# Performance work log

Hardware: AMD Instinct MI355X
Metric: run time of the kernel (lower is better)

## Reference

```python
import jax, jax.numpy as jnp
import numpy as np

IN_CAP_N = 1152   # 128*3*3
IN_CAP_SZ = 5
OUT_CAP_N = 55
OUT_CAP_SZ = 1
BATCH = 8192
ROUTING_ITERS = 2


def setup_inputs() -> dict:
    key = jax.random.key(0)
    k_u, k_w = jax.random.split(key)
    u = jax.random.normal(k_u, (BATCH, IN_CAP_SZ, 128, 3, 3), dtype=jnp.float32)
    W = jax.random.normal(k_w, (1, IN_CAP_N, OUT_CAP_SZ), dtype=jnp.float32)
    b = jnp.zeros((OUT_CAP_N, OUT_CAP_SZ), dtype=jnp.float32)
    return {"u": u, "W": W, "b": b}


def _squash(s):
    # s: (B, 55, 1)
    norm_sq = jnp.sum(s * s, axis=2, keepdims=True)
    norm = jnp.sqrt(norm_sq)
    return norm / (1.0 + norm_sq) * s


def reference(u, W, b):
    B = u.shape[0]
    u_ = u.reshape(B, IN_CAP_SZ, IN_CAP_N)              # (B, 5, 1152)
    u_hat = jnp.matmul(u_, jnp.broadcast_to(W, (B, IN_CAP_N, OUT_CAP_SZ)))  # (B, 5, 1)
    # routing logits, expanded from (55,1) param to (B, 55, 5)
    b_ij = jnp.broadcast_to(b, (B, OUT_CAP_N, IN_CAP_SZ))
    v = None
    for _ in range(ROUTING_ITERS):
        c = jax.nn.softmax(b_ij, axis=1)                 # softmax over out-capsules
        s = jnp.matmul(c, u_hat)                         # (B, 55, 5)@(B, 5, 1) -> (B, 55, 1)
        v = _squash(s)
        b_ij = b_ij + jnp.matmul(v, jnp.swapaxes(u_hat, 1, 2))  # (B, 55, 5)
    return v
```

## Files before the change

kernel.cpp:

```cpp
#include <hip/hip_runtime.h>
#include <math.h>

#define IN_CAP_N   1152
#define IN_CAP_SZ  5
#define OUT_CAP_N  55
#define NBATCH     8192

__global__ __launch_bounds__(320) void digitcaps_kernel(
    const float* __restrict__ u,
    const float* __restrict__ W,
    const float* __restrict__ bparam,
    float* __restrict__ out)
{
    __shared__ float sW[IN_CAP_N];
    __shared__ float s_uhat[IN_CAP_SZ];

    const int tid  = threadIdx.x;
    const int wave = tid >> 6;
    const int lane = tid & 63;
    const int b    = blockIdx.x;

    if (tid < IN_CAP_N / 4) {
        ((float4*)sW)[tid] = ((const float4*)W)[tid];
    }
    __syncthreads();

    const float* urow = u + ((size_t)b * IN_CAP_SZ + wave) * IN_CAP_N;
    float acc = 0.f;
    #pragma unroll
    for (int p = 0; p < 4; ++p) {
        int f = p * 64 + lane;
        float4 uv = ((const float4*)urow)[f];
        float4 wv = ((const float4*)sW)[f];
        acc += uv.x * wv.x + uv.y * wv.y + uv.z * wv.z + uv.w * wv.w;
    }
    if (lane < 32) {
        int f = 256 + lane;
        float4 uv = ((const float4*)urow)[f];
        float4 wv = ((const float4*)sW)[f];
        acc += uv.x * wv.x + uv.y * wv.y + uv.z * wv.z + uv.w * wv.w;
    }
    #pragma unroll
    for (int off = 32; off > 0; off >>= 1)
        acc += __shfl_down(acc, off, 64);
    if (lane == 0) s_uhat[wave] = acc;
    __syncthreads();

    if (wave == 0) {
        float h[IN_CAP_SZ];
        #pragma unroll
        for (int i = 0; i < IN_CAP_SZ; ++i) h[i] = s_uhat[i];

        const bool active = (lane < OUT_CAP_N);
        float binit = active ? bparam[lane] : 0.f;
        float bij[IN_CAP_SZ];
        #pragma unroll
        for (int i = 0; i < IN_CAP_SZ; ++i) bij[i] = binit;

        float v = 0.f;
        #pragma unroll
        for (int it = 0; it < 2; ++it) {
            float c[IN_CAP_SZ];
            #pragma unroll
            for (int i = 0; i < IN_CAP_SZ; ++i) {
                float x = active ? bij[i] : -INFINITY;
                float m = x;
                #pragma unroll
                for (int off = 32; off > 0; off >>= 1)
                    m = fmaxf(m, __shfl_xor(m, off, 64));
                float e = active ? __expf(bij[i] - m) : 0.f;
                float sum = e;
                #pragma unroll
                for (int off = 32; off > 0; off >>= 1)
                    sum += __shfl_xor(sum, off, 64);
                c[i] = e / sum;
            }
            float s = 0.f;
            #pragma unroll
            for (int i = 0; i < IN_CAP_SZ; ++i) s += c[i] * h[i];
            v = fabsf(s) * s / (1.f + s * s);
            #pragma unroll
            for (int i = 0; i < IN_CAP_SZ; ++i) bij[i] += v * h[i];
        }
        if (active) out[(size_t)b * OUT_CAP_N + lane] = v;
    }
}

extern "C" void kernel_launch(void* const* d_in, const int* in_sizes, int n_in,
                              void* d_out, int out_size, void* d_ws, size_t ws_size,
                              hipStream_t stream) {
    const float* u  = (const float*)d_in[0];
    const float* W  = (const float*)d_in[1];
    const float* bp = (const float*)d_in[2];
    float* out = (float*)d_out;
    digitcaps_kernel<<<NBATCH, 320, 0, stream>>>(u, W, bp, out);
}
```

Baseline: 258.1 us.

## Assign one wave per batch element with W held in registers

Each wavefront now handles a whole batch element: it computes all five u_hat dot products with W cached in registers, then runs the routing itself. This removes the LDS staging of W, both block barriers, and the idle waves during routing. The risk is less memory parallelism per batch, since one wave now streams five rows instead of five waves streaming one row each.

```diff
diff --git a/kernel.cpp b/kernel.cpp
--- a/kernel.cpp
+++ b/kernel.cpp
@@ -2,88 +2,83 @@
 #include <math.h>
 
 #define IN_CAP_N   1152
+#define ROW_F4     288
 #define IN_CAP_SZ  5
 #define OUT_CAP_N  55
 #define NBATCH     8192
+#define WAVES_PER_BLOCK 4
 
-__global__ __launch_bounds__(320) void digitcaps_kernel(
+__global__ __launch_bounds__(256) void digitcaps_fused(
     const float* __restrict__ u,
     const float* __restrict__ W,
     const float* __restrict__ bparam,
     float* __restrict__ out)
 {
-    __shared__ float sW[IN_CAP_N];
-    __shared__ float s_uhat[IN_CAP_SZ];
+    const int lane = threadIdx.x & 63;
+    const int wave = threadIdx.x >> 6;
+    const int b    = blockIdx.x * WAVES_PER_BLOCK + wave;
 
-    const int tid  = threadIdx.x;
-    const int wave = tid >> 6;
-    const int lane = tid & 63;
-    const int b    = blockIdx.x;
+    const float4* W4 = (const float4*)W;
+    float4 wreg[5];
+    #pragma unroll
+    for (int p = 0; p < 4; ++p) wreg[p] = W4[p * 64 + lane];
+    wreg[4] = (lane < 32) ? W4[256 + lane] : make_float4(0.f, 0.f, 0.f, 0.f);
 
-    if (tid < IN_CAP_N / 4) {
-        ((float4*)sW)[tid] = ((const float4*)W)[tid];
+    const float4* u4 = (const float4*)(u + (size_t)b * (IN_CAP_SZ * IN_CAP_N));
+    float h[IN_CAP_SZ];
+    #pragma unroll
+    for (int i = 0; i < IN_CAP_SZ; ++i) {
+        const float4* row = u4 + i * ROW_F4;
+        float acc = 0.f;
+        #pragma unroll
+        for (int p = 0; p < 4; ++p) {
+            float4 uv = row[p * 64 + lane];
+            acc += uv.x * wreg[p].x + uv.y * wreg[p].y
+                 + uv.z * wreg[p].z + uv.w * wreg[p].w;
+        }
+        if (lane < 32) {
+            float4 uv = row[256 + lane];
+            acc += uv.x * wreg[4].x + uv.y * wreg[4].y
+                 + uv.z * wreg[4].z + uv.w * wreg[4].w;
+        }
+        #pragma unroll
+        for (int off = 32; off > 0; off >>= 1)
+            acc += __shfl_xor(acc, off, 64);
+        h[i] = acc;
     }
-    __syncthreads();
 
-    const float* urow = u + ((size_t)b * IN_CAP_SZ + wave) * IN_CAP_N;
-    float acc = 0.f;
+    const bool active = (lane < OUT_CAP_N);
+    float binit = active ? bparam[lane] : 0.f;
+    float bij[IN_CAP_SZ];
     #pragma unroll
-    for (int p = 0; p < 4; ++p) {
-        int f = p * 64 + lane;
-        float4 uv = ((const float4*)urow)[f];
-        float4 wv = ((const float4*)sW)[f];
-        acc += uv.x * wv.x + uv.y * wv.y + uv.z * wv.z + uv.w * wv.w;
+    for (int i = 0; i < IN_CAP_SZ; ++i) bij[i] = binit;
+
+    float v = 0.f;
+    #pragma unroll
+    for (int it = 0; it < 2; ++it) {
+        float c[IN_CAP_SZ];
+        #pragma unroll
+        for (int i = 0; i < IN_CAP_SZ; ++i) {
+            float x = active ? bij[i] : -INFINITY;
+            float m = x;
+            #pragma unroll
+            for (int off = 32; off > 0; off >>= 1)
+                m = fmaxf(m, __shfl_xor(m, off, 64));
+            float e = active ? __expf(bij[i] - m) : 0.f;
+            float sum = e;
+            #pragma unroll
+            for (int off = 32; off > 0; off >>= 1)
+                sum += __shfl_xor(sum, off, 64);
+            c[i] = e / sum;
+        }
+        float s = 0.f;
+        #pragma unroll
+        for (int i = 0; i < IN_CAP_SZ; ++i) s += c[i] * h[i];
+        v = fabsf(s) * s / (1.f + s * s);
+        #pragma unroll
+        for (int i = 0; i < IN_CAP_SZ; ++i) bij[i] += v * h[i];
     }
-    if (lane < 32) {
-        int f = 256 + lane;
-        float4 uv = ((const float4*)urow)[f];
-        float4 wv = ((const float4*)sW)[f];
-        acc += uv.x * wv.x + uv.y * wv.y + uv.z * wv.z + uv.w * wv.w;
-    }
-    #pragma unroll
-    for (int off = 32; off > 0; off >>= 1)
-        acc += __shfl_down(acc, off, 64);
-    if (lane == 0) s_uhat[wave] = acc;
-    __syncthreads();
-
-    if (wave == 0) {
-        float h[IN_CAP_SZ];
-        #pragma unroll
-        for (int i = 0; i < IN_CAP_SZ; ++i) h[i] = s_uhat[i];
-
-        const bool active = (lane < OUT_CAP_N);
-        float binit = active ? bparam[lane] : 0.f;
-        float bij[IN_CAP_SZ];
-        #pragma unroll
-        for (int i = 0; i < IN_CAP_SZ; ++i) bij[i] = binit;
-
-        float v = 0.f;
-        #pragma unroll
-        for (int it = 0; it < 2; ++it) {
-            float c[IN_CAP_SZ];
-            #pragma unroll
-            for (int i = 0; i < IN_CAP_SZ; ++i) {
-                float x = active ? bij[i] : -INFINITY;
-                float m = x;
-                #pragma unroll
-                for (int off = 32; off > 0; off >>= 1)
-                    m = fmaxf(m, __shfl_xor(m, off, 64));
-                float e = active ? __expf(bij[i] - m) : 0.f;
-                float sum = e;
-                #pragma unroll
-                for (int off = 32; off > 0; off >>= 1)
-                    sum += __shfl_xor(sum, off, 64);
-                c[i] = e / sum;
-            }
-            float s = 0.f;
-            #pragma unroll
-            for (int i = 0; i < IN_CAP_SZ; ++i) s += c[i] * h[i];
-            v = fabsf(s) * s / (1.f + s * s);
-            #pragma unroll
-            for (int i = 0; i < IN_CAP_SZ; ++i) bij[i] += v * h[i];
-        }
-        if (active) out[(size_t)b * OUT_CAP_N + lane] = v;
-    }
+    if (active) out[(size_t)b * OUT_CAP_N + lane] = v;
 }
 
 extern "C" void kernel_launch(void* const* d_in, const int* in_sizes, int n_in,
@@ -93,5 +88,5 @@
     const float* W  = (const float*)d_in[1];
     const float* bp = (const float*)d_in[2];
     float* out = (float*)d_out;
-    digitcaps_kernel<<<NBATCH, 320, 0, stream>>>(u, W, bp, out);
+    digitcaps_fused<<<NBATCH / WAVES_PER_BLOCK, WAVES_PER_BLOCK * 64, 0, stream>>>(u, W, bp, out);
 }
```

Result: no change. 262.7 us (+1.8%).
